# Performance work log

Hardware: AMD Instinct MI355X
Metric: run time of the kernel (lower is better)

Reference implementation:

```python
import jax, jax.numpy as jnp
import numpy as np

D_MODEL = 1024
N_HEADS = 16
D_K = D_MODEL // N_HEADS
LN_EPS = 1e-5


def setup_inputs() -> dict:
    key = jax.random.key(0)
    ks = jax.random.split(key, 11)
    s = 1.0 / np.sqrt(D_MODEL)
    x = jax.random.normal(ks[0], (4, 2048, D_MODEL), dtype=jnp.float32)
    W_q = jax.random.uniform(ks[1], (D_MODEL, D_MODEL), jnp.float32, -s, s)
    b_q = jax.random.uniform(ks[2], (D_MODEL,), jnp.float32, -s, s)
    W_k = jax.random.uniform(ks[3], (D_MODEL, D_MODEL), jnp.float32, -s, s)
    b_k = jax.random.uniform(ks[4], (D_MODEL,), jnp.float32, -s, s)
    W_v = jax.random.uniform(ks[5], (D_MODEL, D_MODEL), jnp.float32, -s, s)
    b_v = jax.random.uniform(ks[6], (D_MODEL,), jnp.float32, -s, s)
    W_o = jax.random.uniform(ks[7], (D_MODEL, D_MODEL), jnp.float32, -s, s)
    b_o = jax.random.uniform(ks[8], (D_MODEL,), jnp.float32, -s, s)
    ln_gamma = jnp.ones((D_MODEL,), jnp.float32)
    ln_beta = jnp.zeros((D_MODEL,), jnp.float32)
    return {"x": x, "W_q": W_q, "b_q": b_q, "W_k": W_k, "b_k": b_k,
            "W_v": W_v, "b_v": b_v, "W_o": W_o, "b_o": b_o,
            "ln_gamma": ln_gamma, "ln_beta": ln_beta}


def reference(x, W_q, b_q, W_k, b_k, W_v, b_v, W_o, b_o, ln_gamma, ln_beta):
    B, S, D = x.shape
    # Linear projections (torch Linear: x @ W.T + b); split into heads.
    def proj(W, b):
        y = jnp.einsum('bsd,ed->bse', x, W) + b
        return y.reshape(B, S, N_HEADS, D_K).transpose(0, 2, 1, 3)  # [B,H,S,dk]
    Q = proj(W_q, b_q)
    K = proj(W_k, b_k)
    V = proj(W_v, b_v)
    scores = jnp.einsum('bhqd,bhkd->bhqk', Q, K) / np.sqrt(D_K)
    attn = jax.nn.softmax(scores, axis=-1)  # dropout is identity in eval
    context = jnp.einsum('bhqk,bhkd->bhqd', attn, V)
    context = context.transpose(0, 2, 1, 3).reshape(B, S, D)
    out = jnp.einsum('bsd,ed->bse', context, W_o) + b_o
    h = x + out  # residual
    mu = jnp.mean(h, axis=-1, keepdims=True)
    var = jnp.mean(jnp.square(h - mu), axis=-1, keepdims=True)
    return (h - mu) / jnp.sqrt(var + LN_EPS) * ln_gamma + ln_beta
```

## Files before the change

kernel.cpp:

```cpp
#include <hip/hip_runtime.h>
#include <hip/hip_bf16.h>
#include <stdint.h>

typedef __attribute__((ext_vector_type(4))) float f32x4;
typedef __attribute__((ext_vector_type(8))) short bf16x8;
typedef __attribute__((ext_vector_type(4))) short bf16x4;
typedef __attribute__((ext_vector_type(4))) short s16x4;

__device__ __forceinline__ float b2f(short s) {
    union { uint32_t u; float f; } v; v.u = ((uint32_t)(uint16_t)s) << 16; return v.f;
}
__device__ __forceinline__ short f2b(float f) {
    union { float f; uint32_t u; } v; v.f = f;
    uint32_t r = v.u + 0x7FFF + ((v.u >> 16) & 1);
    return (short)(r >> 16);
}
__device__ __forceinline__ f32x4 zero4() { f32x4 z = {0.f, 0.f, 0.f, 0.f}; return z; }

__device__ __forceinline__ void async16(const void* g, void* l) {
    __builtin_amdgcn_global_load_lds(
        (const __attribute__((address_space(1))) void*)g,
        (__attribute__((address_space(3))) void*)l, 16, 0, 0);
}
__device__ __forceinline__ uint32_t lds_addr(const void* p) {
    return (uint32_t)(uintptr_t)(const __attribute__((address_space(3))) void*)p;
}
__device__ __forceinline__ float exp2fast(float x) {
    float r; asm("v_exp_f32 %0, %1" : "=v"(r) : "v"(x)); return r;
}
__device__ __forceinline__ uint32_t cvtpk(float lo, float hi) {
    uint32_t r; asm("v_cvt_pk_bf16_f32 %0, %1, %2" : "=v"(r) : "v"(lo), "v"(hi)); return r;
}

__global__ __launch_bounds__(256)
void cvt5(const float* __restrict__ x,
          const float* __restrict__ wq, const float* __restrict__ wk,
          const float* __restrict__ wv, const float* __restrict__ wo,
          short* __restrict__ xb, short* __restrict__ wqb, short* __restrict__ wkb,
          short* __restrict__ wvb, short* __restrict__ wob)
{
    const int b = blockIdx.x;
    const float* src; short* dst; size_t off;
    if (b < 8192) { src = x; dst = xb; off = (size_t)b * 1024; }
    else {
        const int wsel = (b - 8192) >> 10;
        off = (size_t)((b - 8192) & 1023) * 1024;
        switch (wsel) {
            case 0: src = wq; dst = wqb; break;
            case 1: src = wk; dst = wkb; break;
            case 2: src = wv; dst = wvb; break;
            default: src = wo; dst = wob; break;
        }
    }
    const int t = threadIdx.x;
    const float4 v = *(const float4*)(src + off + t * 4);
    s16x4 o;
    o[0] = f2b(v.x); o[1] = f2b(v.y); o[2] = f2b(v.z); o[3] = f2b(v.w);
    *(s16x4*)(dst + off + t * 4) = o;
}

__global__ __launch_bounds__(256)
void gemm_qkv(const short* __restrict__ A, const short* __restrict__ Wcat,
              const float* __restrict__ bq, const float* __restrict__ bk,
              const float* __restrict__ bv,
              short* __restrict__ Qw, short* __restrict__ Kw, short* __restrict__ Vw)
{
    __shared__ short lsA[128 * 32];
    __shared__ short lsB[128 * 32];
    const int K = 1024;
    const int t = threadIdx.x;
    const int wave = t >> 6, lane = t & 63;
    const int wr = wave >> 1, wc = wave & 1;
    const int lr = lane & 15, kg = lane >> 4;
    const int m0 = blockIdx.y * 128;
    const int nb = blockIdx.x;
    const int tb = nb >> 3;
    const int n0c = (nb & 7) * 128;
    const float* bias = (tb == 0) ? bq : (tb == 1) ? bk : bv;
    short* dst = (tb == 0) ? Qw : (tb == 1) ? Kw : Vw;

    f32x4 acc[4][4];
#pragma unroll
    for (int m = 0; m < 4; ++m)
#pragma unroll
        for (int n = 0; n < 4; ++n) acc[m][n] = zero4();

    const short* Ab = A + (size_t)m0 * K;
    const short* Bb = Wcat + (size_t)nb * 128 * K;
    const int r0 = t >> 2;
    const int c0 = (t & 3) * 8;

    for (int k0 = 0; k0 < K; k0 += 32) {
        __syncthreads();
        async16(Ab + (size_t)r0 * K + k0 + c0,        &lsA[t * 8]);
        async16(Ab + (size_t)(r0 + 64) * K + k0 + c0, &lsA[t * 8 + 2048]);
        async16(Bb + (size_t)r0 * K + k0 + c0,        &lsB[t * 8]);
        async16(Bb + (size_t)(r0 + 64) * K + k0 + c0, &lsB[t * 8 + 2048]);
        __syncthreads();

        bf16x8 aF[4], bF[4];
#pragma unroll
        for (int m = 0; m < 4; ++m)
            aF[m] = *(const bf16x8*)&lsA[(wr * 64 + m * 16 + lr) * 32 + kg * 8];
#pragma unroll
        for (int n = 0; n < 4; ++n)
            bF[n] = *(const bf16x8*)&lsB[(wc * 64 + n * 16 + lr) * 32 + kg * 8];
#pragma unroll
        for (int m = 0; m < 4; ++m)
#pragma unroll
            for (int n = 0; n < 4; ++n)
                acc[m][n] = __builtin_amdgcn_mfma_f32_16x16x32_bf16(aF[m], bF[n], acc[m][n], 0, 0, 0);
    }

#pragma unroll
    for (int n = 0; n < 4; ++n) {
        const int col = n0c + wc * 64 + n * 16 + lr;
        const float bvv = bias[col];
#pragma unroll
        for (int m = 0; m < 4; ++m) {
            const int rowb = m0 + wr * 64 + m * 16 + kg * 4;
#pragma unroll
            for (int r = 0; r < 4; ++r)
                dst[(size_t)(rowb + r) * 1024 + col] = f2b(acc[m][n][r] + bvv);
        }
    }
}

__global__ __launch_bounds__(256)
void gemm_out(const short* __restrict__ A, const short* __restrict__ Bw,
              const float* __restrict__ bias, const float* __restrict__ resid,
              float* __restrict__ C)
{
    __shared__ short lsA[128 * 32];
    __shared__ short lsB[128 * 32];
    const int K = 1024, N = 1024;
    const int t = threadIdx.x;
    const int wave = t >> 6, lane = t & 63;
    const int wr = wave >> 1, wc = wave & 1;
    const int lr = lane & 15, kg = lane >> 4;
    const int m0 = blockIdx.y * 128;
    const int n0 = blockIdx.x * 128;

    f32x4 acc[4][4];
#pragma unroll
    for (int m = 0; m < 4; ++m)
#pragma unroll
        for (int n = 0; n < 4; ++n) acc[m][n] = zero4();

    const short* Ab = A + (size_t)m0 * K;
    const short* Bb = Bw + (size_t)n0 * K;
    const int r0 = t >> 2;
    const int c0 = (t & 3) * 8;

    for (int k0 = 0; k0 < K; k0 += 32) {
        __syncthreads();
        async16(Ab + (size_t)r0 * K + k0 + c0,        &lsA[t * 8]);
        async16(Ab + (size_t)(r0 + 64) * K + k0 + c0, &lsA[t * 8 + 2048]);
        async16(Bb + (size_t)r0 * K + k0 + c0,        &lsB[t * 8]);
        async16(Bb + (size_t)(r0 + 64) * K + k0 + c0, &lsB[t * 8 + 2048]);
        __syncthreads();

        bf16x8 aF[4], bF[4];
#pragma unroll
        for (int m = 0; m < 4; ++m)
            aF[m] = *(const bf16x8*)&lsA[(wr * 64 + m * 16 + lr) * 32 + kg * 8];
#pragma unroll
        for (int n = 0; n < 4; ++n)
            bF[n] = *(const bf16x8*)&lsB[(wc * 64 + n * 16 + lr) * 32 + kg * 8];
#pragma unroll
        for (int m = 0; m < 4; ++m)
#pragma unroll
            for (int n = 0; n < 4; ++n)
                acc[m][n] = __builtin_amdgcn_mfma_f32_16x16x32_bf16(aF[m], bF[n], acc[m][n], 0, 0, 0);
    }

#pragma unroll
    for (int n = 0; n < 4; ++n) {
        const int col = n0 + wc * 64 + n * 16 + lr;
        const float bvv = bias[col];
#pragma unroll
        for (int m = 0; m < 4; ++m) {
            const int rowb = m0 + wr * 64 + m * 16 + kg * 4;
#pragma unroll
            for (int r = 0; r < 4; ++r) {
                const size_t idx = (size_t)(rowb + r) * N + col;
                C[idx] = acc[m][n][r] + bvv + resid[idx];
            }
        }
    }
}

__global__ __launch_bounds__(256)
void attn_fwd(const short* __restrict__ Q, const short* __restrict__ K,
              const short* __restrict__ V, short* __restrict__ ctx)
{
    __shared__ short lsK[2][64 * 64];
    __shared__ short lsV[2][64 * 64];
    __shared__ short lsP[4][32 * 72];

    const float C1 = 0.18033688011112042f;

    const int t = threadIdx.x, w = t >> 6, lane = t & 63;
    const int lr = lane & 15, kg = lane >> 4;
    const int bh = blockIdx.x;
    const size_t base = (size_t)(bh >> 4) * 2048 * 1024 + (size_t)(bh & 15) * 64;
    const short* Qg = Q + base;
    const short* Kg = K + base;
    const short* Vg = V + base;
    short* Og = ctx + base;
    const int q0 = blockIdx.y * 128 + w * 32;

    bf16x8 qB[2][2];
#pragma unroll
    for (int m = 0; m < 2; ++m)
#pragma unroll
        for (int ks = 0; ks < 2; ++ks)
            qB[m][ks] = *(const bf16x8*)(Qg + (size_t)(q0 + m * 16 + lr) * 1024 + ks * 32 + kg * 8);

    const int rK  = t >> 3;
    const int cK  = (((t & 7) ^ (rK & 7))) * 8;
    const int kvV = (t & 127) >> 1;
    const int dV0 = ((t >> 7) << 4) + (t & 1) * 8;
    const int dV1 = dV0 + 32;

    f32x4 o[2][4];
#pragma unroll
    for (int m = 0; m < 2; ++m)
#pragma unroll
        for (int n = 0; n < 4; ++n) o[m][n] = zero4();
    float mx[2] = {-1e30f, -1e30f};
    float lsum[2] = {0.f, 0.f};

    async16(Kg + (size_t)rK * 1024 + cK,        &lsK[0][t * 8]);
    async16(Kg + (size_t)(32 + rK) * 1024 + cK, &lsK[0][t * 8 + 2048]);
    async16(Vg + (size_t)kvV * 1024 + dV0,      &lsV[0][t * 8]);
    async16(Vg + (size_t)kvV * 1024 + dV1,      &lsV[0][t * 8 + 2048]);

    int buf = 0;
    for (int it = 0; it < 32; ++it) {
        __syncthreads();
        if (it + 1 < 32) {
            const int kv0 = (it + 1) * 64;
            short* bK = lsK[buf ^ 1]; short* bV = lsV[buf ^ 1];
            async16(Kg + (size_t)(kv0 + rK) * 1024 + cK,      bK + t * 8);
            async16(Kg + (size_t)(kv0 + 32 + rK) * 1024 + cK, bK + t * 8 + 2048);
            async16(Vg + (size_t)(kv0 + kvV) * 1024 + dV0,    bV + t * 8);
            async16(Vg + (size_t)(kv0 + kvV) * 1024 + dV1,    bV + t * 8 + 2048);
        }
        const short* cbK = lsK[buf];
        const short* cbV = lsV[buf];

        f32x4 s[2][4];
        const int x0 = ((kg)     ^ (lr & 7)) * 8;
        const int x1 = ((4 + kg) ^ (lr & 7)) * 8;
        __builtin_amdgcn_s_setprio(1);
#pragma unroll
        for (int cb = 0; cb < 4; ++cb) {
            const bf16x8 kA0 = *(const bf16x8*)&cbK[(cb * 16 + lr) * 64 + x0];
            const bf16x8 kA1 = *(const bf16x8*)&cbK[(cb * 16 + lr) * 64 + x1];
#pragma unroll
            for (int m = 0; m < 2; ++m) {
                f32x4 a = __builtin_amdgcn_mfma_f32_16x16x32_bf16(kA0, qB[m][0], zero4(), 0, 0, 0);
                s[m][cb] = __builtin_amdgcn_mfma_f32_16x16x32_bf16(kA1, qB[m][1], a, 0, 0, 0);
            }
        }
        __builtin_amdgcn_s_setprio(0);

        float smax[2];
#pragma unroll
        for (int m = 0; m < 2; ++m) {
            float a = fmaxf(fmaxf(s[m][0][0], s[m][0][1]), fmaxf(s[m][0][2], s[m][0][3]));
            float b = fmaxf(fmaxf(s[m][1][0], s[m][1][1]), fmaxf(s[m][1][2], s[m][1][3]));
            float c = fmaxf(fmaxf(s[m][2][0], s[m][2][1]), fmaxf(s[m][2][2], s[m][2][3]));
            float d = fmaxf(fmaxf(s[m][3][0], s[m][3][1]), fmaxf(s[m][3][2], s[m][3][3]));
            float e = fmaxf(fmaxf(a, b), fmaxf(c, d));
            e = fmaxf(e, __shfl_xor(e, 16));
            e = fmaxf(e, __shfl_xor(e, 32));
            smax[m] = e;
        }

        if (!__all((smax[0] <= mx[0] + 64.f) && (smax[1] <= mx[1] + 64.f))) {
            float corrS[2];
#pragma unroll
            for (int m = 0; m < 2; ++m) {
                const float mnew = fmaxf(mx[m], smax[m]);
                corrS[m] = exp2fast((mx[m] - mnew) * C1);
                mx[m] = mnew;
                lsum[m] *= corrS[m];
            }
#pragma unroll
            for (int m = 0; m < 2; ++m) {
                f32x4 c;
#pragma unroll
                for (int r = 0; r < 4; ++r) c[r] = __shfl(corrS[m], kg * 4 + r);
#pragma unroll
                for (int n = 0; n < 4; ++n) {
                    o[m][n][0] *= c[0]; o[m][n][1] *= c[1];
                    o[m][n][2] *= c[2]; o[m][n][3] *= c[3];
                }
            }
        }

#pragma unroll
        for (int m = 0; m < 2; ++m) {
            const float nm2 = mx[m] * C1;
            float tsum = 0.f;
            short* pRow = &lsP[w][(m * 16 + lr) * 72];
#pragma unroll
            for (int cb = 0; cb < 4; ++cb) {
                const float p0 = exp2fast(fmaf(s[m][cb][0], C1, -nm2));
                const float p1 = exp2fast(fmaf(s[m][cb][1], C1, -nm2));
                const float p2 = exp2fast(fmaf(s[m][cb][2], C1, -nm2));
                const float p3 = exp2fast(fmaf(s[m][cb][3], C1, -nm2));
                tsum += (p0 + p1) + (p2 + p3);
                *(uint32_t*)&pRow[cb * 16 + kg * 4]     = cvtpk(p0, p1);
                *(uint32_t*)&pRow[cb * 16 + kg * 4 + 2] = cvtpk(p2, p3);
            }
            tsum += __shfl_xor(tsum, 16);
            tsum += __shfl_xor(tsum, 32);
            lsum[m] += tsum;
        }

        bf16x8 pA[2][2];
#pragma unroll
        for (int m = 0; m < 2; ++m)
#pragma unroll
            for (int kh = 0; kh < 2; ++kh)
                pA[m][kh] = *(const bf16x8*)&lsP[w][(m * 16 + lr) * 72 + kh * 32 + kg * 8];

        bf16x4 tv[4][4];
#pragma unroll
        for (int n = 0; n < 4; ++n) {
            const uint32_t a = lds_addr(&cbV[n * 1024 + kg * 128 + lr]);
            asm volatile(
                "ds_read_b64_tr_b16 %0, %4\n\t"
                "ds_read_b64_tr_b16 %1, %4 offset:128\n\t"
                "ds_read_b64_tr_b16 %2, %4 offset:1024\n\t"
                "ds_read_b64_tr_b16 %3, %4 offset:1152"
                : "=&v"(tv[n][0]), "=&v"(tv[n][1]), "=&v"(tv[n][2]), "=&v"(tv[n][3])
                : "v"(a));
        }
        asm volatile("s_waitcnt lgkmcnt(0)" ::: "memory");
        __builtin_amdgcn_sched_barrier(0);

        __builtin_amdgcn_s_setprio(1);
#pragma unroll
        for (int n = 0; n < 4; ++n) {
#pragma unroll
            for (int kh = 0; kh < 2; ++kh) {
                const bf16x8 vB = __builtin_shufflevector(tv[n][kh * 2], tv[n][kh * 2 + 1],
                                                          0, 1, 2, 3, 4, 5, 6, 7);
#pragma unroll
                for (int m = 0; m < 2; ++m)
                    o[m][n] = __builtin_amdgcn_mfma_f32_16x16x32_bf16(pA[m][kh], vB, o[m][n], 0, 0, 0);
            }
        }
        __builtin_amdgcn_s_setprio(0);
        buf ^= 1;
    }

#pragma unroll
    for (int m = 0; m < 2; ++m) {
        f32x4 inv;
#pragma unroll
        for (int r = 0; r < 4; ++r) inv[r] = 1.0f / __shfl(lsum[m], kg * 4 + r);
#pragma unroll
        for (int n = 0; n < 4; ++n)
#pragma unroll
            for (int r = 0; r < 4; ++r) {
                const int row = q0 + m * 16 + kg * 4 + r;
                Og[(size_t)row * 1024 + n * 16 + lr] = f2b(o[m][n][r] * inv[r]);
            }
    }
}

__global__ __launch_bounds__(256)
void ln_inplace(float* __restrict__ io, const float* __restrict__ gamma,
                const float* __restrict__ beta)
{
    __shared__ float redS[4];
    __shared__ float redQ[4];
    const int t = threadIdx.x, wave = t >> 6, lane = t & 63;
    const size_t rb = (size_t)blockIdx.x * 1024;

    float4 v4 = *(const float4*)&io[rb + t * 4];
    float v[4] = {v4.x, v4.y, v4.z, v4.w};

    float s = 0.f, sq = 0.f;
#pragma unroll
    for (int j = 0; j < 4; ++j) { s += v[j]; sq += v[j] * v[j]; }
#pragma unroll
    for (int off = 32; off; off >>= 1) {
        s  += __shfl_xor(s, off);
        sq += __shfl_xor(sq, off);
    }
    if (lane == 0) { redS[wave] = s; redQ[wave] = sq; }
    __syncthreads();
    const float mean = (redS[0] + redS[1] + redS[2] + redS[3]) * (1.0f / 1024.0f);
    const float ex2  = (redQ[0] + redQ[1] + redQ[2] + redQ[3]) * (1.0f / 1024.0f);
    const float var  = fmaxf(ex2 - mean * mean, 0.f);
    const float inv  = rsqrtf(var + 1e-5f);

    float4 o4;
    o4.x = (v[0] - mean) * inv * gamma[t * 4 + 0] + beta[t * 4 + 0];
    o4.y = (v[1] - mean) * inv * gamma[t * 4 + 1] + beta[t * 4 + 1];
    o4.z = (v[2] - mean) * inv * gamma[t * 4 + 2] + beta[t * 4 + 2];
    o4.w = (v[3] - mean) * inv * gamma[t * 4 + 3] + beta[t * 4 + 3];
    *(float4*)&io[rb + t * 4] = o4;
}

extern "C" void kernel_launch(void* const* d_in, const int* in_sizes, int n_in,
                              void* d_out, int out_size, void* d_ws, size_t ws_size,
                              hipStream_t stream)
{
    const float* x  = (const float*)d_in[0];
    const float* Wq = (const float*)d_in[1];
    const float* bq = (const float*)d_in[2];
    const float* Wk = (const float*)d_in[3];
    const float* bk = (const float*)d_in[4];
    const float* Wv = (const float*)d_in[5];
    const float* bv = (const float*)d_in[6];
    const float* Wo = (const float*)d_in[7];
    const float* bo = (const float*)d_in[8];
    const float* gamma = (const float*)d_in[9];
    const float* beta  = (const float*)d_in[10];

    const size_t NX = (size_t)8192 * 1024;
    const size_t NW = (size_t)1024 * 1024;

    short* xb  = (short*)d_ws;
    short* Wqb = xb + NX;
    short* Wkb = Wqb + NW;
    short* Wvb = Wkb + NW;
    short* Wob = Wvb + NW;
    short* Qw  = Wob + NW;
    short* Kw  = Qw + NX;
    short* Vw  = Kw + NX;
    short* Cw  = Vw + NX;
    float* out = (float*)d_out;

    dim3 blk(256);
    cvt5<<<dim3(12288), blk, 0, stream>>>(x, Wq, Wk, Wv, Wo, xb, Wqb, Wkb, Wvb, Wob);
    gemm_qkv<<<dim3(24, 64), blk, 0, stream>>>(xb, Wqb, bq, bk, bv, Qw, Kw, Vw);
    attn_fwd<<<dim3(64, 16), blk, 0, stream>>>(Qw, Kw, Vw, Cw);
    gemm_out<<<dim3(8, 64), blk, 0, stream>>>(Cw, Wob, bo, x, out);
    ln_inplace<<<dim3(8192), blk, 0, stream>>>(out, gamma, beta);
}
```

Baseline: 241.6 us.

## Share GEMM core with 64-wide swizzled K tiles; interleave attention softmax with PV

Both projection GEMMs now go through one templated core that loads 64-wide K slices into XOR-swizzled LDS tiles. This halves the number of barrier-bounded iterations and is meant to avoid LDS bank conflicts. In attention, each wave's P buffer shrinks to 16 rows with an XOR swizzle and is processed per m-tile, so exp/pack for one tile can overlap the MFMAs of the other. The costs are double the LDS per GEMM block, which may lower occupancy, and possibly more serialization between the per-tile LDS write and read in attention.

```diff
diff --git a/kernel.cpp b/kernel.cpp
--- a/kernel.cpp
+++ b/kernel.cpp
@@ -59,71 +59,90 @@
     *(s16x4*)(dst + off + t * 4) = o;
 }
 
+template <bool OUTF32, bool RESID>
+__device__ __forceinline__
+void gemm_core(const short* __restrict__ Ab, const short* __restrict__ Bb,
+               const float* __restrict__ bias, const float* __restrict__ resid,
+               void* __restrict__ Cv, int m0, int n0col, int K, int N,
+               short* lsA, short* lsB)
+{
+    const int t = threadIdx.x;
+    const int wave = t >> 6, lane = t & 63;
+    const int wr = wave >> 1, wc = wave & 1;
+    const int lr = lane & 15, kg = lane >> 4;
+
+    f32x4 acc[4][4];
+#pragma unroll
+    for (int m = 0; m < 4; ++m)
+#pragma unroll
+        for (int n = 0; n < 4; ++n) acc[m][n] = zero4();
+
+    const int rG = t >> 3;
+    const int cG = (((t & 7) ^ (rG & 7))) * 8;
+
+    for (int k0 = 0; k0 < K; k0 += 64) {
+        __syncthreads();
+#pragma unroll
+        for (int i = 0; i < 4; ++i) {
+            async16(Ab + (size_t)(rG + 32 * i) * K + k0 + cG, &lsA[t * 8 + 2048 * i]);
+            async16(Bb + (size_t)(rG + 32 * i) * K + k0 + cG, &lsB[t * 8 + 2048 * i]);
+        }
+        __syncthreads();
+
+#pragma unroll
+        for (int ks = 0; ks < 2; ++ks) {
+            const int xc = ((ks * 4 + kg) ^ (lr & 7)) * 8;
+            bf16x8 aF[4], bF[4];
+#pragma unroll
+            for (int m = 0; m < 4; ++m)
+                aF[m] = *(const bf16x8*)&lsA[(wr * 64 + m * 16 + lr) * 64 + xc];
+#pragma unroll
+            for (int n = 0; n < 4; ++n)
+                bF[n] = *(const bf16x8*)&lsB[(wc * 64 + n * 16 + lr) * 64 + xc];
+#pragma unroll
+            for (int m = 0; m < 4; ++m)
+#pragma unroll
+                for (int n = 0; n < 4; ++n)
+                    acc[m][n] = __builtin_amdgcn_mfma_f32_16x16x32_bf16(aF[m], bF[n], acc[m][n], 0, 0, 0);
+        }
+    }
+
+#pragma unroll
+    for (int n = 0; n < 4; ++n) {
+        const int col = n0col + wc * 64 + n * 16 + lr;
+        const float bvv = bias[col - n0col + n0col];
+#pragma unroll
+        for (int m = 0; m < 4; ++m) {
+            const int rowb = m0 + wr * 64 + m * 16 + kg * 4;
+#pragma unroll
+            for (int r = 0; r < 4; ++r) {
+                const size_t idx = (size_t)(rowb + r) * N + col;
+                float v = acc[m][n][r] + bvv;
+                if (RESID) v += resid[idx];
+                if (OUTF32) ((float*)Cv)[idx] = v;
+                else        ((short*)Cv)[idx] = f2b(v);
+            }
+        }
+    }
+}
+
 __global__ __launch_bounds__(256)
 void gemm_qkv(const short* __restrict__ A, const short* __restrict__ Wcat,
               const float* __restrict__ bq, const float* __restrict__ bk,
               const float* __restrict__ bv,
               short* __restrict__ Qw, short* __restrict__ Kw, short* __restrict__ Vw)
 {
-    __shared__ short lsA[128 * 32];
-    __shared__ short lsB[128 * 32];
-    const int K = 1024;
-    const int t = threadIdx.x;
-    const int wave = t >> 6, lane = t & 63;
-    const int wr = wave >> 1, wc = wave & 1;
-    const int lr = lane & 15, kg = lane >> 4;
-    const int m0 = blockIdx.y * 128;
+    __shared__ short lsA[128 * 64];
+    __shared__ short lsB[128 * 64];
     const int nb = blockIdx.x;
     const int tb = nb >> 3;
-    const int n0c = (nb & 7) * 128;
     const float* bias = (tb == 0) ? bq : (tb == 1) ? bk : bv;
     short* dst = (tb == 0) ? Qw : (tb == 1) ? Kw : Vw;
-
-    f32x4 acc[4][4];
-#pragma unroll
-    for (int m = 0; m < 4; ++m)
-#pragma unroll
-        for (int n = 0; n < 4; ++n) acc[m][n] = zero4();
-
-    const short* Ab = A + (size_t)m0 * K;
-    const short* Bb = Wcat + (size_t)nb * 128 * K;
-    const int r0 = t >> 2;
-    const int c0 = (t & 3) * 8;
-
-    for (int k0 = 0; k0 < K; k0 += 32) {
-        __syncthreads();
-        async16(Ab + (size_t)r0 * K + k0 + c0,        &lsA[t * 8]);
-        async16(Ab + (size_t)(r0 + 64) * K + k0 + c0, &lsA[t * 8 + 2048]);
-        async16(Bb + (size_t)r0 * K + k0 + c0,        &lsB[t * 8]);
-        async16(Bb + (size_t)(r0 + 64) * K + k0 + c0, &lsB[t * 8 + 2048]);
-        __syncthreads();
-
-        bf16x8 aF[4], bF[4];
-#pragma unroll
-        for (int m = 0; m < 4; ++m)
-            aF[m] = *(const bf16x8*)&lsA[(wr * 64 + m * 16 + lr) * 32 + kg * 8];
-#pragma unroll
-        for (int n = 0; n < 4; ++n)
-            bF[n] = *(const bf16x8*)&lsB[(wc * 64 + n * 16 + lr) * 32 + kg * 8];
-#pragma unroll
-        for (int m = 0; m < 4; ++m)
-#pragma unroll
-            for (int n = 0; n < 4; ++n)
-                acc[m][n] = __builtin_amdgcn_mfma_f32_16x16x32_bf16(aF[m], bF[n], acc[m][n], 0, 0, 0);
-    }
-
-#pragma unroll
-    for (int n = 0; n < 4; ++n) {
-        const int col = n0c + wc * 64 + n * 16 + lr;
-        const float bvv = bias[col];
-#pragma unroll
-        for (int m = 0; m < 4; ++m) {
-            const int rowb = m0 + wr * 64 + m * 16 + kg * 4;
-#pragma unroll
-            for (int r = 0; r < 4; ++r)
-                dst[(size_t)(rowb + r) * 1024 + col] = f2b(acc[m][n][r] + bvv);
-        }
-    }
+    gemm_core<false, false>(A + (size_t)blockIdx.y * 128 * 1024,
+                            Wcat + (size_t)nb * 128 * 1024,
+                            bias - (nb & 7) * 128,
+                            nullptr, dst, blockIdx.y * 128, (nb & 7) * 128, 1024, 1024,
+                            lsA, lsB);
 }
 
 __global__ __launch_bounds__(256)
@@ -131,63 +150,12 @@
               const float* __restrict__ bias, const float* __restrict__ resid,
               float* __restrict__ C)
 {
-    __shared__ short lsA[128 * 32];
-    __shared__ short lsB[128 * 32];
-    const int K = 1024, N = 1024;
-    const int t = threadIdx.x;
-    const int wave = t >> 6, lane = t & 63;
-    const int wr = wave >> 1, wc = wave & 1;
-    const int lr = lane & 15, kg = lane >> 4;
-    const int m0 = blockIdx.y * 128;
-    const int n0 = blockIdx.x * 128;
-
-    f32x4 acc[4][4];
-#pragma unroll
-    for (int m = 0; m < 4; ++m)
-#pragma unroll
-        for (int n = 0; n < 4; ++n) acc[m][n] = zero4();
-
-    const short* Ab = A + (size_t)m0 * K;
-    const short* Bb = Bw + (size_t)n0 * K;
-    const int r0 = t >> 2;
-    const int c0 = (t & 3) * 8;
-
-    for (int k0 = 0; k0 < K; k0 += 32) {
-        __syncthreads();
-        async16(Ab + (size_t)r0 * K + k0 + c0,        &lsA[t * 8]);
-        async16(Ab + (size_t)(r0 + 64) * K + k0 + c0, &lsA[t * 8 + 2048]);
-        async16(Bb + (size_t)r0 * K + k0 + c0,        &lsB[t * 8]);
-        async16(Bb + (size_t)(r0 + 64) * K + k0 + c0, &lsB[t * 8 + 2048]);
-        __syncthreads();
-
-        bf16x8 aF[4], bF[4];
-#pragma unroll
-        for (int m = 0; m < 4; ++m)
-            aF[m] = *(const bf16x8*)&lsA[(wr * 64 + m * 16 + lr) * 32 + kg * 8];
-#pragma unroll
-        for (int n = 0; n < 4; ++n)
-            bF[n] = *(const bf16x8*)&lsB[(wc * 64 + n * 16 + lr) * 32 + kg * 8];
-#pragma unroll
-        for (int m = 0; m < 4; ++m)
-#pragma unroll
-            for (int n = 0; n < 4; ++n)
-                acc[m][n] = __builtin_amdgcn_mfma_f32_16x16x32_bf16(aF[m], bF[n], acc[m][n], 0, 0, 0);
-    }
-
-#pragma unroll
-    for (int n = 0; n < 4; ++n) {
-        const int col = n0 + wc * 64 + n * 16 + lr;
-        const float bvv = bias[col];
-#pragma unroll
-        for (int m = 0; m < 4; ++m) {
-            const int rowb = m0 + wr * 64 + m * 16 + kg * 4;
-#pragma unroll
-            for (int r = 0; r < 4; ++r) {
-                const size_t idx = (size_t)(rowb + r) * N + col;
-                C[idx] = acc[m][n][r] + bvv + resid[idx];
-            }
-        }
-    }
+    __shared__ short lsA[128 * 64];
+    __shared__ short lsB[128 * 64];
+    gemm_core<true, true>(A + (size_t)blockIdx.y * 128 * 1024,
+                          Bw + (size_t)blockIdx.x * 128 * 1024,
+                          bias, resid, C, blockIdx.y * 128, blockIdx.x * 128, 1024, 1024,
+                          lsA, lsB);
 }
 
 __global__ __launch_bounds__(256)
@@ -196,7 +164,7 @@
 {
     __shared__ short lsK[2][64 * 64];
     __shared__ short lsV[2][64 * 64];
-    __shared__ short lsP[4][32 * 72];
+    __shared__ short lsP[4][16 * 64];
 
     const float C1 = 0.18033688011112042f;
 
@@ -230,6 +198,9 @@
         for (int n = 0; n < 4; ++n) o[m][n] = zero4();
     float mx[2] = {-1e30f, -1e30f};
     float lsum[2] = {0.f, 0.f};
+
+    const int pmask = (lr & 7) << 3;
+    short* lsPw = lsP[w];
 
     async16(Kg + (size_t)rK * 1024 + cK,        &lsK[0][t * 8]);
     async16(Kg + (size_t)(32 + rK) * 1024 + cK, &lsK[0][t * 8 + 2048]);
@@ -301,33 +272,6 @@
             }
         }
 
-#pragma unroll
-        for (int m = 0; m < 2; ++m) {
-            const float nm2 = mx[m] * C1;
-            float tsum = 0.f;
-            short* pRow = &lsP[w][(m * 16 + lr) * 72];
-#pragma unroll
-            for (int cb = 0; cb < 4; ++cb) {
-                const float p0 = exp2fast(fmaf(s[m][cb][0], C1, -nm2));
-                const float p1 = exp2fast(fmaf(s[m][cb][1], C1, -nm2));
-                const float p2 = exp2fast(fmaf(s[m][cb][2], C1, -nm2));
-                const float p3 = exp2fast(fmaf(s[m][cb][3], C1, -nm2));
-                tsum += (p0 + p1) + (p2 + p3);
-                *(uint32_t*)&pRow[cb * 16 + kg * 4]     = cvtpk(p0, p1);
-                *(uint32_t*)&pRow[cb * 16 + kg * 4 + 2] = cvtpk(p2, p3);
-            }
-            tsum += __shfl_xor(tsum, 16);
-            tsum += __shfl_xor(tsum, 32);
-            lsum[m] += tsum;
-        }
-
-        bf16x8 pA[2][2];
-#pragma unroll
-        for (int m = 0; m < 2; ++m)
-#pragma unroll
-            for (int kh = 0; kh < 2; ++kh)
-                pA[m][kh] = *(const bf16x8*)&lsP[w][(m * 16 + lr) * 72 + kh * 32 + kg * 8];
-
         bf16x4 tv[4][4];
 #pragma unroll
         for (int n = 0; n < 4; ++n) {
@@ -343,19 +287,42 @@
         asm volatile("s_waitcnt lgkmcnt(0)" ::: "memory");
         __builtin_amdgcn_sched_barrier(0);
 
-        __builtin_amdgcn_s_setprio(1);
-#pragma unroll
-        for (int n = 0; n < 4; ++n) {
-#pragma unroll
-            for (int kh = 0; kh < 2; ++kh) {
-                const bf16x8 vB = __builtin_shufflevector(tv[n][kh * 2], tv[n][kh * 2 + 1],
-                                                          0, 1, 2, 3, 4, 5, 6, 7);
-#pragma unroll
-                for (int m = 0; m < 2; ++m)
-                    o[m][n] = __builtin_amdgcn_mfma_f32_16x16x32_bf16(pA[m][kh], vB, o[m][n], 0, 0, 0);
-            }
-        }
-        __builtin_amdgcn_s_setprio(0);
+#pragma unroll
+        for (int m = 0; m < 2; ++m) {
+            const float nm2 = mx[m] * C1;
+            float tsum = 0.f;
+#pragma unroll
+            for (int cb = 0; cb < 4; ++cb) {
+                const float p0 = exp2fast(fmaf(s[m][cb][0], C1, -nm2));
+                const float p1 = exp2fast(fmaf(s[m][cb][1], C1, -nm2));
+                const float p2 = exp2fast(fmaf(s[m][cb][2], C1, -nm2));
+                const float p3 = exp2fast(fmaf(s[m][cb][3], C1, -nm2));
+                tsum += (p0 + p1) + (p2 + p3);
+                const int c0i = (cb * 16 + kg * 4) ^ pmask;
+                *(uint32_t*)&lsPw[lr * 64 + c0i]     = cvtpk(p0, p1);
+                *(uint32_t*)&lsPw[lr * 64 + c0i + 2] = cvtpk(p2, p3);
+            }
+            tsum += __shfl_xor(tsum, 16);
+            tsum += __shfl_xor(tsum, 32);
+            lsum[m] += tsum;
+
+            bf16x8 pA[2];
+#pragma unroll
+            for (int kh = 0; kh < 2; ++kh)
+                pA[kh] = *(const bf16x8*)&lsPw[lr * 64 + ((kh * 32 + kg * 8) ^ pmask)];
+
+            __builtin_amdgcn_s_setprio(1);
+#pragma unroll
+            for (int n = 0; n < 4; ++n) {
+#pragma unroll
+                for (int kh = 0; kh < 2; ++kh) {
+                    const bf16x8 vB = __builtin_shufflevector(tv[n][kh * 2], tv[n][kh * 2 + 1],
+                                                              0, 1, 2, 3, 4, 5, 6, 7);
+                    o[m][n] = __builtin_amdgcn_mfma_f32_16x16x32_bf16(pA[kh], vB, o[m][n], 0, 0, 0);
+                }
+            }
+            __builtin_amdgcn_s_setprio(0);
+        }
         buf ^= 1;
     }
 
```

Result: no change. 240.9 us (-0.3%).
